# Optimization experiments

Hardware: AMD Instinct MI355X
Metric: run time of the kernel (lower is better)

The kernel has to match this reference:

```python
import jax, jax.numpy as jnp
import numpy as np

# ---- geometry constants (from init_kwargs) ----
GRID = (160, 160, 160)
ORIGIN = np.array([-160.0, -160.0, -160.0], dtype=np.float32)   # corner of image volume (mm)
VOXSIZE = np.array([2.0, 2.0, 2.0], dtype=np.float32)           # mm
TIME_RES = 300.0   # ps (FWHM-like timing resolution)
TOF_BIN = 10.0     # ps
C_HALF = 0.15      # speed of light / 2 in mm/ps -> converts TOF time to position along LOR
NSTEPS = 256       # fixed ray-march samples per LOR (jit-friendly surrogate for Siddon stepping)
N_LORS = 100000
EPS = 1e-8

SIGMA = jnp.float32(TIME_RES * C_HALF / 2.355)  # spatial TOF sigma (mm), FWHM -> sigma
NVOX = GRID[0] * GRID[1] * GRID[2]
STRIDES = np.array([GRID[1] * GRID[2], GRID[2], 1], dtype=np.int32)


def setup_inputs() -> dict:
    key = jax.random.key(0)
    k1, k2, k3, k4, k5 = jax.random.split(key, 5)
    image = jax.random.uniform(k1, GRID, dtype=jnp.float32)
    effmap = jax.random.uniform(k2, GRID, dtype=jnp.float32) + 0.5
    # LOR endpoints on a cylinder of radius 250 mm surrounding the 320 mm FOV
    R = 250.0
    ang = jax.random.uniform(k3, (N_LORS, 2), dtype=jnp.float32) * (2.0 * np.pi)
    z = jax.random.uniform(k4, (N_LORS, 2), dtype=jnp.float32) * 300.0 - 150.0
    p0 = jnp.stack([R * jnp.cos(ang[:, 0]), R * jnp.sin(ang[:, 0]), z[:, 0]], axis=-1)
    p1 = jnp.stack([-R * jnp.cos(ang[:, 1]), -R * jnp.sin(ang[:, 1]), z[:, 1]], axis=-1)
    tof = jax.random.normal(k5, (N_LORS, 1), dtype=jnp.float32) * 100.0  # ps
    lors = jnp.concatenate([p0, p1, tof], axis=-1)  # [N,7]
    return {"image": image, "effmap": effmap, "lors": lors}


def _trace(lors):
    """Ray-march samples, flat voxel indices, and TOF-weighted per-sample lengths."""
    p0, p1, tof = lors[:, 0:3], lors[:, 3:6], lors[:, 6]
    d = p1 - p0                                   # [N,3]
    L = jnp.linalg.norm(d, axis=-1)               # [N]
    dl = L / NSTEPS                               # [N] step length (mm)
    t = (jnp.arange(NSTEPS, dtype=jnp.float32) + 0.5) / NSTEPS   # [S]
    pts = p0[:, None, :] + t[None, :, None] * d[:, None, :]      # [N,S,3]
    idx = jnp.floor((pts - ORIGIN) / VOXSIZE).astype(jnp.int32)  # [N,S,3]
    inb = jnp.all((idx >= 0) & (idx < jnp.array(GRID, dtype=jnp.int32)), axis=-1)  # [N,S]
    flat = jnp.sum(jnp.clip(idx, 0, jnp.array(GRID, dtype=jnp.int32) - 1)
                   * jnp.asarray(STRIDES), axis=-1)              # [N,S]
    # TOF Gaussian weight along the ray, centered at midpoint + tof offset
    s = (t[None, :] - 0.5) * L[:, None]           # signed distance from midpoint (mm)
    s_tof = (tof * C_HALF)[:, None]
    w = jnp.exp(-0.5 * jnp.square((s - s_tof) / SIGMA))
    w = jnp.where(inb, w, 0.0) * dl[:, None]      # [N,S] intersection-length weight
    return flat, w


def reference(image, effmap, lors):
    flat, w = _trace(lors)                        # [N,S], [N,S]
    img_flat = image.reshape(-1)
    # projection: p[n] = sum_s w[n,s] * image[voxel(n,s)]
    p = jnp.sum(jnp.take(img_flat, flat) * w, axis=1)            # [N]
    # backprojection of lor_values=p: bp[v] = sum_{n,s: voxel=v} w[n,s] * p[n]
    bp = jnp.zeros((NVOX,), dtype=image.dtype).at[flat.reshape(-1)].add(
        (p[:, None] * w).reshape(-1)).reshape(GRID)
    return image / (effmap + EPS) * bp
```

## Files before the change

### kernel.cpp

```cpp
#include <hip/hip_runtime.h>
#include <math.h>

#define NSTEPS 256
#define GRIDN  160
#define NVOX   (160 * 160 * 160)
#define NTPA   20
#define NTILES (NTPA * NTPA * NTPA)
#define ITEM_CAP (4 * 1024 * 1024)
#define MAXSEG 64

#define INV_SIGMA 0.05233333f

struct LorT { float4 a; float4 b; };

__device__ __forceinline__ bool sample_vox(
    int j, float p0x, float p0y, float p0z,
    float dx, float dy, float dz, float L, float s_tof,
    int& ix, int& iy, int& iz, float& e)
{
#pragma clang fp contract(off)
    const float t = (j + 0.5f) * (1.0f / 256.0f);
    const float px = p0x + t * dx;
    const float py = p0y + t * dy;
    const float pz = p0z + t * dz;
    const float fx = floorf((px + 160.0f) * 0.5f);
    const float fy = floorf((py + 160.0f) * 0.5f);
    const float fz = floorf((pz + 160.0f) * 0.5f);
    const bool inb = (fx >= 0.0f) & (fx < 160.0f) &
                     (fy >= 0.0f) & (fy < 160.0f) &
                     (fz >= 0.0f) & (fz < 160.0f);
    const float s = (t - 0.5f) * L;
    const float u = (s - s_tof) * INV_SIGMA;
    e = 0.5f * (u * u);
    if (inb & (e < 10.0f)) {
        ix = (int)fx; iy = (int)fy; iz = (int)fz;
        return true;
    }
    return false;
}

__device__ __forceinline__ void lor_window(
    float p0x, float p0y, float p0z, float dx, float dy, float dz,
    float L, float s_tof, int& j0, int& j1)
{
#pragma clang fp contract(off)
    const float SIGMA = (float)(45.0 / 2.355);
    const float CUTS  = 4.4721360f * SIGMA;
    const float invL = 1.0f / L;
    float t0 = 0.5f + (s_tof - CUTS) * invL;
    float t1 = 0.5f + (s_tof + CUTS) * invL;
    if (t0 > t1) { const float tmp = t0; t0 = t1; t1 = tmp; }
    const float pc[3] = {p0x, p0y, p0z};
    const float dc[3] = {dx, dy, dz};
    #pragma unroll
    for (int a = 0; a < 3; ++a) {
        if (dc[a] != 0.0f) {
            const float inv = 1.0f / dc[a];
            const float ta = (-160.0f - pc[a]) * inv;
            const float tb = ( 160.0f - pc[a]) * inv;
            t0 = fmaxf(t0, fminf(ta, tb));
            t1 = fminf(t1, fmaxf(ta, tb));
        } else if (pc[a] < -160.0f || pc[a] >= 160.0f) t1 = -1.0f;
    }
    t0 = fmaxf(t0, 0.0f);
    t1 = fminf(t1, 1.0f);
    j0 = (int)floorf(t0 * 256.0f - 0.5f) - 2;
    j1 = (int)ceilf (t1 * 256.0f - 0.5f) + 2;
    if (!(t0 <= t1)) { j0 = 0; j1 = -1; }
    j0 = max(j0, 0);
    j1 = min(j1, NSTEPS - 1);
}

__global__ __launch_bounds__(256) void emit_kernel(
    const float* __restrict__ image,
    const float* __restrict__ lors, LorT* __restrict__ lortab,
    int* __restrict__ histcur, unsigned* __restrict__ items,
    float* __restrict__ p,
    unsigned* __restrict__ items_raw, int* __restrict__ nseg,
    int n, int phase)
{
#pragma clang fp contract(off)
    const int wave = (int)((blockIdx.x * blockDim.x + threadIdx.x) >> 6);
    const int lane = threadIdx.x & 63;
    if (wave >= n) return;

    float p0x, p0y, p0z, tof, dx, dy, dz, L;
    if (phase == 0) {
        const float* l = lors + (size_t)wave * 7;
        p0x = l[0]; p0y = l[1]; p0z = l[2];
        dx = l[3] - p0x; dy = l[4] - p0y; dz = l[5] - p0z; tof = l[6];
        L = sqrtf(dx * dx + dy * dy + dz * dz);
        if (lane == 0) {
            lortab[wave].a = make_float4(p0x, p0y, p0z, tof);
            lortab[wave].b = make_float4(dx, dy, dz, L);
        }
    } else {
        const float4 A = lortab[wave].a, B = lortab[wave].b;
        p0x = A.x; p0y = A.y; p0z = A.z; tof = A.w;
        dx  = B.x; dy  = B.y; dz  = B.z; L   = B.w;
    }
    const float s_tof = tof * 0.15f;
    const float dl = L * (1.0f / 256.0f);
    int j0, j1;
    lor_window(p0x, p0y, p0z, dx, dy, dz, L, s_tof, j0, j1);
    const int nk = (j1 - j0 + 64) >> 6;

    float psum = 0.0f;
    int running = 0;
    for (int k = 0; k < nk; ++k) {
        const int j = j0 + lane + (k << 6);
        int ix, iy, iz; float e;
        const bool valid = (j <= j1) &&
            sample_vox(j, p0x, p0y, p0z, dx, dy, dz, L, s_tof, ix, iy, iz, e);
        if (phase == 0) {
            if (valid)
                psum += image[ix * 25600 + iy * 160 + iz] * (__expf(-e) * dl);
        }
        const unsigned key = valid
            ? (unsigned)((ix >> 3) * 400 + (iy >> 3) * 20 + (iz >> 3))
            : 0xFFFFFFFFu;
        const unsigned prev = __shfl_up(key, 1, 64);
        const bool chg = (lane == 0) || (prev != key);
        const unsigned long long cm = __ballot(chg);
        const unsigned long long segmask = __ballot(chg && valid);
        if (chg && valid) {
            const unsigned long long above = cm & ~((2ULL << lane) - 1ULL);
            const int nxt = above ? (__ffsll((unsigned long long)above) - 1) : 64;
            const int len = nxt - lane;
            if (phase == 0) {
                const int tr = atomicAdd(&histcur[key], 1);
                if (items_raw) {
                    const int rankb =
                        (int)__popcll(segmask & ((1ULL << lane) - 1ULL));
                    const int si = running + rankb;
                    if (si < MAXSEG)
                        items_raw[(size_t)wave * MAXSEG + si] =
                            ((unsigned)tr << 14) | ((unsigned)j << 6)
                            | (unsigned)(len - 1);
                }
            } else {
                const int slot = atomicAdd(&histcur[key], 1);
                if (slot < ITEM_CAP)
                    items[slot] = ((unsigned)wave << 14) | ((unsigned)j << 6)
                                | (unsigned)(len - 1);
            }
        }
        running += (int)__popcll(segmask);
    }
    if (phase == 0) {
        #pragma unroll
        for (int off = 32; off >= 1; off >>= 1) psum += __shfl_xor(psum, off, 64);
        if (lane == 0) {
            p[wave] = psum;
            if (nseg) nseg[wave] = min(running, MAXSEG);
        }
    }
}

__global__ __launch_bounds__(256) void scatter_kernel(
    const LorT* __restrict__ lortab, const unsigned* __restrict__ items_raw,
    const int* __restrict__ nseg, const int* __restrict__ offs,
    unsigned* __restrict__ items, int n)
{
#pragma clang fp contract(off)
    const int wave = (int)((blockIdx.x * blockDim.x + threadIdx.x) >> 6);
    const int lane = threadIdx.x & 63;
    if (wave >= n) return;
    const int ns = nseg[wave];
    if (ns == 0) return;
    const float4 A = lortab[wave].a, B = lortab[wave].b;
    const float s_tof = A.w * 0.15f;
    for (int s = lane; s < ns; s += 64) {
        const unsigned it32 = items_raw[(size_t)wave * MAXSEG + s];
        const int j = (int)((it32 >> 6) & 255);
        int ix = 0, iy = 0, iz = 0; float e;
        sample_vox(j, A.x, A.y, A.z, B.x, B.y, B.z, B.w, s_tof, ix, iy, iz, e);
        const unsigned key =
            (unsigned)((ix >> 3) * 400 + (iy >> 3) * 20 + (iz >> 3));
        const int slot = offs[key] + (int)(it32 >> 14);
        if (slot < ITEM_CAP)
            items[slot] = ((unsigned)wave << 14) | (it32 & 0x3FFFu);
    }
}

__global__ __launch_bounds__(1024) void scan_kernel(
    const int* __restrict__ hist, int* __restrict__ offs, int* __restrict__ cursor)
{
    __shared__ int part[1024];
    const int t = threadIdx.x;
    const int base = t * 8;
    int loc[8]; int s = 0;
    #pragma unroll
    for (int i = 0; i < 8; ++i) {
        const int h = (base + i < NTILES) ? hist[base + i] : 0;
        loc[i] = s; s += h;
    }
    part[t] = s;
    __syncthreads();
    for (int off = 1; off < 1024; off <<= 1) {
        int v = 0;
        if (t >= off) v = part[t - off];
        __syncthreads();
        part[t] += v;
        __syncthreads();
    }
    const int excl = (t > 0) ? part[t - 1] : 0;
    #pragma unroll
    for (int i = 0; i < 8; ++i) {
        if (base + i < NTILES) {
            offs[base + i]   = excl + loc[i];
            cursor[base + i] = excl + loc[i];
        }
    }
    if (t == 1023) offs[NTILES] = part[1023];
}

__global__ __launch_bounds__(256) void tileB_kernel(
    const float* __restrict__ image, const float* __restrict__ effmap,
    const LorT* __restrict__ lortab, const int* __restrict__ offs,
    const unsigned* __restrict__ items, const float* __restrict__ p,
    float* __restrict__ out)
{
    const int b = blockIdx.x;
    const int i0 = offs[b], i1 = min(offs[b + 1], ITEM_CAP);
    if (i0 >= i1) return;
    const int tx0 = (b / 400) << 3, ty0 = ((b / 20) % 20) << 3, tz0 = (b % 20) << 3;
    __shared__ float acc[512];
    const int t = threadIdx.x;
    for (int v = t; v < 512; v += 256) acc[v] = 0.0f;
    __syncthreads();
    for (int idx = i0 + t; idx < i1; idx += 256) {
        const unsigned it = items[idx];
        const int lor = (int)(it >> 14);
        const int js  = (int)((it >> 6) & 255);
        const int len = (int)(it & 63) + 1;
        const float4 A = lortab[lor].a, B = lortab[lor].b;
        const float dl = B.w * (1.0f / 256.0f);
        const float s_tof = A.w * 0.15f;
        const float pv = p[lor];
        for (int m = 0; m < len; ++m) {
            int ix, iy, iz; float e;
            if (sample_vox(js + m, A.x, A.y, A.z, B.x, B.y, B.z, B.w, s_tof,
                           ix, iy, iz, e)) {
                const int lx = ix - tx0, ly = iy - ty0, lz = iz - tz0;
                if ((unsigned)lx < 8u && (unsigned)ly < 8u && (unsigned)lz < 8u)
                    atomicAdd(&acc[(lx << 6) | (ly << 3) | lz],
                              pv * (__expf(-e) * dl));
            }
        }
    }
    __syncthreads();
    for (int v = t; v < 512; v += 256) {
        const int lx = v >> 6, ly = (v >> 3) & 7, lz = v & 7;
        const size_t g = (size_t)(tx0 + lx) * 25600 + (ty0 + ly) * 160 + (tz0 + lz);
        out[g] = image[g] / (effmap[g] + 1e-8f) * acc[v];
    }
}

__global__ __launch_bounds__(256) void trace_direct_kernel(
    const float* __restrict__ image, const float* __restrict__ lors,
    float* __restrict__ bp, int n_lors)
{
#pragma clang fp contract(off)
    const int wave = (int)((blockIdx.x * blockDim.x + threadIdx.x) >> 6);
    const int lane = threadIdx.x & 63;
    if (wave >= n_lors) return;
    const float* l = lors + (size_t)wave * 7;
    const float p0x = l[0], p0y = l[1], p0z = l[2];
    const float dx = l[3] - p0x, dy = l[4] - p0y, dz = l[5] - p0z;
    const float tof = l[6];
    const float L  = sqrtf(dx * dx + dy * dy + dz * dz);
    const float dl = L * (1.0f / 256.0f);
    const float s_tof = tof * 0.15f;
    int j0, j1;
    lor_window(p0x, p0y, p0z, dx, dy, dz, L, s_tof, j0, j1);
    const int nk = (j1 - j0 + 64) >> 6;
    if (nk <= 0) return;
    int flat[4]; float w[4]; float psum = 0.0f;
    for (int k = 0; k < nk; ++k) {
        const int j = j0 + lane + (k << 6);
        int ix, iy, iz; float e; float wk = 0.0f; int fl = 0;
        if (j <= j1 &&
            sample_vox(j, p0x, p0y, p0z, dx, dy, dz, L, s_tof, ix, iy, iz, e)) {
            wk = __expf(-e) * dl;
            fl = ix * 25600 + iy * 160 + iz;
            psum += image[fl] * wk;
        }
        flat[k] = fl; w[k] = wk;
    }
    #pragma unroll
    for (int off = 32; off >= 1; off >>= 1) psum += __shfl_xor(psum, off, 64);
    for (int k = 0; k < nk; ++k)
        if (w[k] > 0.0f) atomicAdd(&bp[flat[k]], psum * w[k]);
}

__global__ __launch_bounds__(256) void finalize_kernel(
    const float4* __restrict__ image, const float4* __restrict__ effmap,
    float4* __restrict__ out, int n4)
{
    const int i = blockIdx.x * blockDim.x + threadIdx.x;
    if (i >= n4) return;
    const float4 im = image[i];
    const float4 ef = effmap[i];
    float4 b = out[i];
    b.x = im.x / (ef.x + 1e-8f) * b.x;
    b.y = im.y / (ef.y + 1e-8f) * b.y;
    b.z = im.z / (ef.z + 1e-8f) * b.z;
    b.w = im.w / (ef.w + 1e-8f) * b.w;
    out[i] = b;
}

extern "C" void kernel_launch(void* const* d_in, const int* in_sizes, int n_in,
                              void* d_out, int out_size, void* d_ws, size_t ws_size,
                              hipStream_t stream) {
    const float* image  = (const float*)d_in[0];
    const float* effmap = (const float*)d_in[1];
    const float* lors   = (const float*)d_in[2];
    float* out = (float*)d_out;
    const int n = in_sizes[2] / 7;

    char* ws = (char*)d_ws;
    const size_t hist_off   = 0;
    const size_t offs_off   = hist_off + 32768;
    const size_t cursor_off = offs_off + 32768;
    const size_t p_off      = cursor_off + 32768;
    const size_t lortab_off = p_off + (((size_t)n * 4 + 255) & ~(size_t)255);
    const size_t nseg_off   = lortab_off + (size_t)n * sizeof(LorT);
    const size_t raw_off    = nseg_off + (((size_t)n * 4 + 255) & ~(size_t)255);
    const size_t items_off  = raw_off + (((size_t)n * MAXSEG * 4 + 255) & ~(size_t)255);
    const size_t total_stg  = items_off + (size_t)ITEM_CAP * 4;
    const size_t items_off2 = nseg_off;
    const size_t total_nostg = items_off2 + (size_t)ITEM_CAP * 4;

    hipMemsetAsync(out, 0, (size_t)NVOX * sizeof(float), stream);

    if (ws_size >= total_stg && n < (1 << 17)) {
        int*      hist   = (int*)(ws + hist_off);
        int*      offs   = (int*)(ws + offs_off);
        int*      cursor = (int*)(ws + cursor_off);
        float*    p      = (float*)(ws + p_off);
        LorT*     lortab = (LorT*)(ws + lortab_off);
        int*      nseg   = (int*)(ws + nseg_off);
        unsigned* items_raw = (unsigned*)(ws + raw_off);
        unsigned* items  = (unsigned*)(ws + items_off);

        hipMemsetAsync(hist, 0, NTILES * sizeof(int), stream);

        const int blocksE = (n + 3) / 4;
        emit_kernel<<<blocksE, 256, 0, stream>>>(image, lors, lortab, hist, items,
                                                 p, items_raw, nseg, n, 0);
        scan_kernel<<<1, 1024, 0, stream>>>(hist, offs, cursor);
        scatter_kernel<<<blocksE, 256, 0, stream>>>(lortab, items_raw, nseg,
                                                    offs, items, n);
        tileB_kernel<<<NTILES, 256, 0, stream>>>(image, effmap, lortab, offs, items,
                                                 p, out);
    } else if (ws_size >= total_nostg && n < (1 << 17)) {
        int*      hist   = (int*)(ws + hist_off);
        int*      offs   = (int*)(ws + offs_off);
        int*      cursor = (int*)(ws + cursor_off);
        float*    p      = (float*)(ws + p_off);
        LorT*     lortab = (LorT*)(ws + lortab_off);
        unsigned* items  = (unsigned*)(ws + items_off2);

        hipMemsetAsync(hist, 0, NTILES * sizeof(int), stream);

        const int blocksE = (n + 3) / 4;
        emit_kernel<<<blocksE, 256, 0, stream>>>(image, lors, lortab, hist, items,
                                                 p, nullptr, nullptr, n, 0);
        scan_kernel<<<1, 1024, 0, stream>>>(hist, offs, cursor);
        emit_kernel<<<blocksE, 256, 0, stream>>>(image, lors, lortab, cursor, items,
                                                 p, nullptr, nullptr, n, 1);
        tileB_kernel<<<NTILES, 256, 0, stream>>>(image, effmap, lortab, offs, items,
                                                 p, out);
    } else {
        trace_direct_kernel<<<(n + 3) / 4, 256, 0, stream>>>(image, lors, out, n);
        const int n4 = NVOX / 4;
        finalize_kernel<<<(n4 + 255) / 256, 256, 0, stream>>>(
            (const float4*)image, (const float4*)effmap, (float4*)out, n4);
    }
}
```

Baseline: 215.6 us.

## Load-balance tile backprojection by flattening item segments into per-sample work

In the tile backprojection kernel, each thread used to walk a whole variable-length segment of samples, which left threads in a wave idle while the longest segment finished. Now each batch of 256 items is staged in shared memory along with its LOR data. A block-wide prefix scan over segment lengths is computed, and threads then take individual samples found by binary search over the scan. This evens out the work across lanes, at the cost of extra shared memory, many __syncthreads in the scan, and a binary search per sample.

```diff
diff --git a/kernel.cpp b/kernel.cpp
--- a/kernel.cpp
+++ b/kernel.cpp
@@ -225,29 +225,60 @@
     const int i0 = offs[b], i1 = min(offs[b + 1], ITEM_CAP);
     if (i0 >= i1) return;
     const int tx0 = (b / 400) << 3, ty0 = ((b / 20) % 20) << 3, tz0 = (b % 20) << 3;
-    __shared__ float acc[512];
+    __shared__ float  acc[512];
+    __shared__ int    pfx[256];
+    __shared__ unsigned sit[256];
+    __shared__ float4 sA[256], sB[256];
+    __shared__ float  sp[256];
     const int t = threadIdx.x;
     for (int v = t; v < 512; v += 256) acc[v] = 0.0f;
-    __syncthreads();
-    for (int idx = i0 + t; idx < i1; idx += 256) {
-        const unsigned it = items[idx];
-        const int lor = (int)(it >> 14);
-        const int js  = (int)((it >> 6) & 255);
-        const int len = (int)(it & 63) + 1;
-        const float4 A = lortab[lor].a, B = lortab[lor].b;
-        const float dl = B.w * (1.0f / 256.0f);
-        const float s_tof = A.w * 0.15f;
-        const float pv = p[lor];
-        for (int m = 0; m < len; ++m) {
+
+    for (int base = i0; base < i1; base += 256) {
+        const int cnt = min(256, i1 - base);
+        int len = 0;
+        unsigned it = 0;
+        if (t < cnt) {
+            it = items[base + t];
+            len = (int)(it & 63) + 1;
+            const int lor = (int)(it >> 14);
+            sA[t] = lortab[lor].a;
+            sB[t] = lortab[lor].b;
+            sp[t] = p[lor];
+        }
+        sit[t] = it;
+        pfx[t] = len;
+        __syncthreads();
+        #pragma unroll
+        for (int off = 1; off < 256; off <<= 1) {
+            const int v = (t >= off) ? pfx[t - off] : 0;
+            __syncthreads();
+            pfx[t] += v;
+            __syncthreads();
+        }
+        const int S = pfx[cnt - 1];
+        for (int s = t; s < S; s += 256) {
+            int lo = 0, hi = cnt - 1;
+            #pragma unroll
+            while (lo < hi) {
+                const int mid = (lo + hi) >> 1;
+                if (pfx[mid] > s) hi = mid; else lo = mid + 1;
+            }
+            const unsigned w = sit[lo];
+            const int m  = s - ((lo > 0) ? pfx[lo - 1] : 0);
+            const int js = (int)((w >> 6) & 255);
+            const float4 A = sA[lo], B = sB[lo];
+            const float dl = B.w * (1.0f / 256.0f);
+            const float s_tof = A.w * 0.15f;
             int ix, iy, iz; float e;
             if (sample_vox(js + m, A.x, A.y, A.z, B.x, B.y, B.z, B.w, s_tof,
                            ix, iy, iz, e)) {
                 const int lx = ix - tx0, ly = iy - ty0, lz = iz - tz0;
                 if ((unsigned)lx < 8u && (unsigned)ly < 8u && (unsigned)lz < 8u)
                     atomicAdd(&acc[(lx << 6) | (ly << 3) | lz],
-                              pv * (__expf(-e) * dl));
+                              sp[lo] * (__expf(-e) * dl));
             }
         }
+        __syncthreads();
     }
     __syncthreads();
     for (int v = t; v < 512; v += 256) {
```

New measurement: 227.4 us. +5.5%, slower.
